# Kernel optimization log

Measured on AMD Instinct MI355X. Metric: run time of the kernel, lower is better.

## Reference

```python
import jax, jax.numpy as jnp
import numpy as np

DIM = 768
NUM_HEADS = 12
HEAD_DIM = DIM // NUM_HEADS
SCALE = HEAD_DIM ** -0.5
EPS = 1e-6


def setup_inputs() -> dict:
    key = jax.random.key(0)
    k_x, k_p, k_qkv, k_proj = jax.random.split(key, 4)
    B, N = 16, 577
    x = jax.random.normal(k_x, (B, N, DIM), dtype=jnp.float32)
    # binary keep/drop policy per token (as produced by an upstream gumbel gate)
    policy = jax.random.randint(k_p, (B, N, 1), 0, 2).astype(jnp.float32)
    Wqkv = jax.random.normal(k_qkv, (DIM, 3 * DIM), dtype=jnp.float32) * 0.02
    bqkv = jnp.zeros((3 * DIM,), dtype=jnp.float32)
    Wproj = jax.random.normal(k_proj, (DIM, DIM), dtype=jnp.float32) * 0.02
    bproj = jnp.zeros((DIM,), dtype=jnp.float32)
    return {"x": x, "policy": policy, "Wqkv": Wqkv, "bqkv": bqkv,
            "Wproj": Wproj, "bproj": bproj}


def reference(x, policy, Wqkv, bqkv, Wproj, bproj):
    B, N, C = x.shape
    # qkv projection -> [3, B, H, N, Dh]
    qkv = (x @ Wqkv + bqkv).reshape(B, N, 3, NUM_HEADS, HEAD_DIM)
    qkv = jnp.transpose(qkv, (2, 0, 3, 1, 4))
    q, k, v = qkv[0], qkv[1], qkv[2]
    # scaled attention logits [B, H, N, N]
    attn = jnp.einsum("bhnd,bhmd->bhnm", q, k) * SCALE
    # policy-masked softmax (training-mode formula: eye keeps self-attention alive)
    ap = policy.reshape(B, 1, 1, N)
    eye = jnp.eye(N, dtype=ap.dtype).reshape(1, 1, N, N)
    ap = ap + (1.0 - ap) * eye
    max_att = jnp.max(attn, axis=-1, keepdims=True)
    e = jnp.exp(attn - max_att) * ap
    attn = (e + EPS / N) / (jnp.sum(e, axis=-1, keepdims=True) + EPS)
    # attend and project
    out = jnp.einsum("bhnm,bhmd->bhnd", attn, v)
    out = jnp.transpose(out, (0, 2, 1, 3)).reshape(B, N, C)
    return out @ Wproj + bproj
```

## Files before the change

kernel.cpp:

```cpp
#include <hip/hip_runtime.h>
#include <hip/hip_bf16.h>

#define QKVC   2304
#define NHEAD  12
#define NTOK   577
#define NBATCH 16
#define NROWS  (NBATCH * NTOK)
#define NPAD   640
#define SCALE  0.125f
#define EPSV   1e-6f
#define KT     24
#define CH     512

typedef __bf16  bf16x8 __attribute__((ext_vector_type(8)));
typedef float   f32x4  __attribute__((ext_vector_type(4)));

__device__ __forceinline__ unsigned short f2bf(float f) {
    union { float f; unsigned u; } v; v.f = f;
    unsigned r = v.u + 0x7FFFu + ((v.u >> 16) & 1u);
    return (unsigned short)(r >> 16);
}
__device__ __forceinline__ unsigned short f2bf_trunc(float f) {
    return (unsigned short)(__float_as_uint(f) >> 16);
}
__device__ __forceinline__ unsigned pack2bf(float a, float b) {
    return (unsigned)f2bf(a) | ((unsigned)f2bf(b) << 16);
}
__device__ __forceinline__ f32x4 mfma16(bf16x8 a, bf16x8 b, f32x4 c) {
    return __builtin_amdgcn_mfma_f32_16x16x32_bf16(a, b, c, 0, 0, 0);
}

#define GLDS16(g, l) __builtin_amdgcn_global_load_lds( \
    (const __attribute__((address_space(1))) unsigned int*)(g), \
    (__attribute__((address_space(3))) unsigned int*)(l), 16, 0, 0)


__device__ void transpose_tile(const float* __restrict__ src, unsigned short* __restrict__ dst,
                               int N, int bx, int by, int t) {
    __shared__ unsigned short lt[64 * 72];
    int n0 = bx * 64, k0 = by * 64;
    int kk = t >> 4, nn = (t & 15) * 4;
    for (int i = 0; i < 4; i++) {
        int kr = kk + i * 16;
        float4 v = *(const float4*)&src[(size_t)(k0 + kr) * N + n0 + nn];
        lt[(nn + 0) * 72 + kr] = f2bf(v.x);
        lt[(nn + 1) * 72 + kr] = f2bf(v.y);
        lt[(nn + 2) * 72 + kr] = f2bf(v.z);
        lt[(nn + 3) * 72 + kr] = f2bf(v.w);
    }
    __syncthreads();
    int n = t >> 2;
    int ks = (t & 3) * 16;
    int gn = n0 + n;
    int ntile = gn >> 4, r = gn & 15, s = (r >> 1) & 3;
    for (int j = 0; j < 2; j++) {
        int k = k0 + ks + j * 8;
        int kt = k >> 5;
        int q = ((k >> 3) & 3) ^ s;
        uint4 v = *(uint4*)&lt[n * 72 + ks + j * 8];
        *(uint4*)&dst[((size_t)ntile * KT + kt) * CH + r * 32 + q * 8] = v;
    }
}

#define NCHUNK (577 * KT)
#define CONVB  ((NCHUNK + 15) / 16)
__global__ void k_prep(const float* __restrict__ x, unsigned short* __restrict__ xbt,
                       const float* __restrict__ Wqkv, unsigned short* __restrict__ wqkvt,
                       const float* __restrict__ Wproj, unsigned short* __restrict__ wprojt) {
    int id = blockIdx.x, t = threadIdx.x;
    if (id < CONVB) {
        int cid = id * 16 + (t >> 4);
        if (cid < NCHUNK) {
            int r = t & 15;
            int mt = cid / KT, kt = cid - mt * KT;
            const float* src = x + ((size_t)mt * 16 + r) * 768 + kt * 32;
            int s = (r >> 1) & 3;
            unsigned short* dst = xbt + (size_t)cid * CH + r * 32;
            #pragma unroll
            for (int q = 0; q < 4; q++) {
                int g = q ^ s;
                float4 v0 = *(const float4*)(src + g * 8);
                float4 v1 = *(const float4*)(src + g * 8 + 4);
                uint4 u;
                u.x = pack2bf(v0.x, v0.y);
                u.y = pack2bf(v0.z, v0.w);
                u.z = pack2bf(v1.x, v1.y);
                u.w = pack2bf(v1.z, v1.w);
                *(uint4*)(dst + q * 8) = u;
            }
        }
    } else if (id < CONVB + 432) {
        int i2 = id - CONVB;
        transpose_tile(Wqkv, wqkvt, QKVC, i2 % 36, i2 / 36, t);
    } else {
        int i2 = id - CONVB - 432;
        transpose_tile(Wproj, wprojt, 768, i2 % 12, i2 / 12, t);
    }
}

template <bool F32OUT>
__global__ __launch_bounds__(512, 2)
void k_gemm(const unsigned short* __restrict__ A, const unsigned short* __restrict__ B,
            const float* __restrict__ bias, void* __restrict__ outp, int Ncols,
            unsigned short* __restrict__ vt) {
    __shared__ unsigned short SL[36864];
    int t = threadIdx.x;
    int lane = t & 63, wave = t >> 6, quad = lane >> 4, l15 = lane & 15;
    int wm = wave >> 2, wn = wave & 3;
    int nT = Ncols >> 7;
    int nwg = gridDim.x;

    int q8 = nwg >> 3, r8 = nwg & 7;
    int xcd = blockIdx.x & 7, idx = blockIdx.x >> 3;
    int wg = (xcd < r8 ? xcd * (q8 + 1) : r8 * (q8 + 1) + (xcd - r8) * q8) + idx;
    int m0 = (wg / nT) * 256;
    int n0 = (wg % nT) * 128;

    const unsigned short* gA0 = A + ((size_t)((m0 >> 4) + wave) * KT) * CH + lane * 8;
    const unsigned short* gA1 = gA0 + (size_t)8 * KT * CH;
    const unsigned short* gB0 = B + ((size_t)((n0 >> 4) + wave) * KT) * CH + lane * 8;

    f32x4 acc[8][2] = {};

    auto STAGE = [&](int sx, unsigned slot) {
        unsigned sa = slot * 8192u + (unsigned)wave * 512u;
        unsigned sb = 24576u + slot * 4096u + (unsigned)wave * 512u;
        GLDS16(gA0 + sx * CH, &SL[sa]);
        GLDS16(gA1 + sx * CH, &SL[sa + 4096]);
        GLDS16(gB0 + sx * CH, &SL[sb]);
    };

    unsigned ro = (unsigned)(quad ^ ((l15 >> 1) & 3)) * 8u;

    auto STEP = [&](unsigned slot, int sx, unsigned sslot, bool stage) {
        unsigned ab = slot * 8192u;
        unsigned bb = 24576u + slot * 4096u;
        if (stage) STAGE(sx, sslot);
        bf16x8 b0 = *(const bf16x8*)&SL[bb + (unsigned)(wn * 32 + l15) * 32u + ro];
        bf16x8 b1 = *(const bf16x8*)&SL[bb + (unsigned)(wn * 32 + 16 + l15) * 32u + ro];
        __builtin_amdgcn_s_setprio(1);
        #pragma unroll
        for (int mi = 0; mi < 8; mi++) {
            bf16x8 a = *(const bf16x8*)&SL[ab + (unsigned)(wm * 128 + mi * 16 + l15) * 32u + ro];
            acc[mi][0] = mfma16(a, b0, acc[mi][0]);
            acc[mi][1] = mfma16(a, b1, acc[mi][1]);
        }
        __builtin_amdgcn_s_setprio(0);
    };

    STAGE(0, 0); STAGE(1, 1);
    for (int s = 0; s < 23; s++) {
        asm volatile("s_waitcnt vmcnt(3)" ::: "memory");
        asm volatile("s_barrier" ::: "memory");
        STEP((unsigned)(s % 3), s + 2, (unsigned)((s + 2) % 3), s < 22);
    }
    asm volatile("s_waitcnt vmcnt(0)" ::: "memory");
    asm volatile("s_barrier" ::: "memory");
    STEP(2u, 0, 0u, false);

    if constexpr (F32OUT) {
        for (int ni = 0; ni < 2; ni++) {
            int col = n0 + wn * 32 + ni * 16 + l15;
            float bv = bias[col];
            for (int mi = 0; mi < 8; mi++) {
                int rowm = m0 + wm * 128 + mi * 16 + quad * 4;
                for (int r = 0; r < 4; r++) {
                    int m = rowm + r;
                    if (m < NROWS)
                        ((float*)outp)[(size_t)m * Ncols + col] = acc[mi][ni][r] + bv;
                }
            }
        }
    } else {
        __syncthreads();
        for (int ni = 0; ni < 2; ni++) {
            int colL = wn * 32 + ni * 16 + l15;
            float bv = bias[n0 + colL];
            for (int mi = 0; mi < 8; mi++) {
                int rowL = wm * 128 + mi * 16 + quad * 4;
                for (int r = 0; r < 4; r++)
                    SL[(rowL + r) * 136 + colL] = f2bf(acc[mi][ni][r] + bv);
            }
        }
        __syncthreads();
        if (n0 < 1536) {
            for (int rr = 0; rr < 8; rr++) {
                int row = rr * 32 + (t >> 4);
                int m = m0 + row;
                if (m < NROWS) {
                    uint4 v = *(uint4*)&SL[row * 136 + (t & 15) * 8];
                    *(uint4*)&((unsigned short*)outp)[(size_t)m * Ncols + n0 + (t & 15) * 8] = v;
                }
            }
        } else {
            int h0 = (n0 - 1536) >> 6;
            for (int i = 0; i < 16; i++) {
                int c = wave * 16 + i;
                int h = h0 + (c >> 6), d = c & 63;
                for (int half = 0; half < 4; half++) {
                    int lr = half * 64 + lane;
                    int m = m0 + lr;
                    if (m < NROWS) {
                        unsigned bbx = (unsigned)m / 577u;
                        int tok = m - (int)bbx * 577;
                        vt[(((size_t)bbx * NHEAD + h) * 64 + d) * NPAD + tok] =
                            SL[lr * 136 + c];
                    }
                }
            }
        }
    }
}

__global__ __launch_bounds__(256, 4)
void k_attn(const unsigned short* __restrict__ qkv, const unsigned short* __restrict__ vt,
            const float* __restrict__ policy, unsigned short* __restrict__ ao) {
    __shared__ unsigned short Ks[64 * 72];
    __shared__ unsigned short Vs[64 * 72];
    __shared__ unsigned short Ps[4][32 * 72];
    __shared__ float pol[NPAD];
    int t = threadIdx.x;
    int lane = t & 63, wave = t >> 6, quad = lane >> 4, l15 = lane & 15;
    int b = blockIdx.z, h = blockIdx.y, qt = blockIdx.x;
    const unsigned short* qbase = qkv + (size_t)(b * NTOK) * QKVC + h * 64;
    const unsigned short* kbase = qkv + (size_t)(b * NTOK) * QKVC + 768 + h * 64;
    const unsigned short* vbase = vt + (size_t)(b * NHEAD + h) * 64 * NPAD;

    for (int i = t; i < NPAD; i += 256)
        pol[i] = (i < NTOK) ? policy[b * NTOK + i] : 0.f;

    bf16x8 qf[2][2];
    for (int mi = 0; mi < 2; mi++) {
        const unsigned short* qp =
            qbase + (size_t)(qt * 128 + mi * 64 + wave * 16 + l15) * QKVC + quad * 8;
        qf[mi][0] = *(const bf16x8*)qp;
        qf[mi][1] = *(const bf16x8*)(qp + 32);
    }
    bf16x8 onesf;
    for (int j = 0; j < 8; j++) onesf[j] = (__bf16)1.0f;
    f32x4 o[2][4] = {};
    f32x4 ls[2] = {};
    int rowtok0[2];
    for (int mi = 0; mi < 2; mi++)
        rowtok0[mi] = qt * 128 + mi * 64 + wave * 16 + quad * 4;
    __syncthreads();

    for (int kt = 0; kt < 10; kt++) {
        int key0 = kt * 64;
        for (int i = t; i < 512; i += 256) {
            int row = i >> 3, seg = (i & 7) * 8;
            *(uint4*)&Ks[row * 72 + seg] = *(const uint4*)&kbase[(size_t)(key0 + row) * QKVC + seg];
            *(uint4*)&Vs[row * 72 + seg] = *(const uint4*)&vbase[(size_t)row * NPAD + key0 + seg];
        }
        __syncthreads();

        for (int ci = 0; ci < 4; ci++) {
            bf16x8 kf0 = *(const bf16x8*)&Ks[(ci * 16 + l15) * 72 + quad * 8];
            bf16x8 kf1 = *(const bf16x8*)&Ks[(ci * 16 + l15) * 72 + 32 + quad * 8];
            int col = key0 + ci * 16 + l15;
            float pc = pol[col];
            for (int mi = 0; mi < 2; mi++) {
                f32x4 a = {};
                a = mfma16(qf[mi][0], kf0, a);
                a = mfma16(qf[mi][1], kf1, a);
                for (int r = 0; r < 4; r++) {
                    float ap = (col == rowtok0[mi] + r) ? 1.f : pc;
                    float e = __expf(a[r] * SCALE) * ap;
                    Ps[wave][(mi * 16 + quad * 4 + r) * 72 + ci * 16 + l15] = f2bf_trunc(e);
                }
            }
        }
        __asm__ volatile("s_waitcnt lgkmcnt(0)" ::: "memory");
        bf16x8 pf[2][2];
        for (int mi = 0; mi < 2; mi++) {
            pf[mi][0] = *(const bf16x8*)&Ps[wave][(mi * 16 + l15) * 72 + quad * 8];
            pf[mi][1] = *(const bf16x8*)&Ps[wave][(mi * 16 + l15) * 72 + 32 + quad * 8];
            ls[mi] = mfma16(pf[mi][0], onesf, ls[mi]);
            ls[mi] = mfma16(pf[mi][1], onesf, ls[mi]);
        }
        for (int di = 0; di < 4; di++) {
            bf16x8 vf0 = *(const bf16x8*)&Vs[(di * 16 + l15) * 72 + quad * 8];
            bf16x8 vf1 = *(const bf16x8*)&Vs[(di * 16 + l15) * 72 + 32 + quad * 8];
            for (int mi = 0; mi < 2; mi++) {
                o[mi][di] = mfma16(pf[mi][0], vf0, o[mi][di]);
                o[mi][di] = mfma16(pf[mi][1], vf1, o[mi][di]);
            }
        }
        __syncthreads();
    }

    for (int mi = 0; mi < 2; mi++) {
        for (int r = 0; r < 4; r++) {
            int tok = rowtok0[mi] + r;
            if (tok < NTOK) {
                float inv = __builtin_amdgcn_rcpf(ls[mi][r] + EPSV);
                int m = b * NTOK + tok;
                int mt = m >> 4, rr = m & 15, s = (rr >> 1) & 3;
                unsigned short* dst = ao + ((size_t)mt * KT) * CH + rr * 32;
                for (int di = 0; di < 4; di++) {
                    int k = h * 64 + di * 16 + l15;
                    int kt2 = k >> 5;
                    int q = ((k >> 3) & 3) ^ s;
                    dst[(size_t)kt2 * CH + q * 8 + (l15 & 7)] =
                        f2bf(o[mi][di][r] * inv);
                }
            }
        }
    }
}

extern "C" void kernel_launch(void* const* d_in, const int* in_sizes, int n_in,
                              void* d_out, int out_size, void* d_ws, size_t ws_size,
                              hipStream_t stream) {
    const float* x      = (const float*)d_in[0];
    const float* policy = (const float*)d_in[1];
    const float* Wqkv   = (const float*)d_in[2];
    const float* bqkv   = (const float*)d_in[3];
    const float* Wproj  = (const float*)d_in[4];
    const float* bproj  = (const float*)d_in[5];
    float* out = (float*)d_out;

    unsigned short* p = (unsigned short*)d_ws;
    unsigned short* xb     = p;
    unsigned short* ao     = p; p += (size_t)NROWS * 768;
    unsigned short* wqkvt  = p; p += (size_t)QKVC * 768;
    unsigned short* wprojt = p; p += (size_t)768 * 768;
    unsigned short* qkvb   = p; p += (size_t)NROWS * QKVC;
    unsigned short* vt     = p; p += (size_t)NBATCH * NHEAD * 64 * NPAD;

    int mT = (NROWS + 255) / 256;

    k_prep<<<CONVB + 432 + 144, 256, 0, stream>>>(x, xb, Wqkv, wqkvt, Wproj, wprojt);
    k_gemm<false><<<mT * (QKVC / 128), 512, 0, stream>>>(
        xb, wqkvt, bqkv, (void*)qkvb, QKVC, vt);
    k_attn<<<dim3(NPAD / 128, NHEAD, NBATCH), 256, 0, stream>>>(qkvb, vt, policy, ao);
    k_gemm<true><<<mT * (768 / 128), 512, 0, stream>>>(
        ao, wprojt, bproj, (void*)out, 768, nullptr);
}
```

Measured before the change: 193.1 us.

## Enlarge GEMM tile to 256x256 with 4-phase split-K double-buffered pipeline

The GEMM block tile grows from 256x128 to 256x256, with K staged two sub-chunks at a time into 128KB of double-buffered LDS. Each K step is split into four quadrant phases that interleave global-to-LDS prefetch with MFMA work. The aim is to raise arithmetic intensity and halve B/A reload traffic per output. In exchange the block uses the full LDS and more accumulators, which drops occupancy to one block per CU, and the grid gets smaller, which may hurt load balance (the projection GEMM has only 3 column tiles).

```diff
diff --git a/kernel.cpp b/kernel.cpp
--- a/kernel.cpp
+++ b/kernel.cpp
@@ -103,108 +103,145 @@
 void k_gemm(const unsigned short* __restrict__ A, const unsigned short* __restrict__ B,
             const float* __restrict__ bias, void* __restrict__ outp, int Ncols,
             unsigned short* __restrict__ vt) {
-    __shared__ unsigned short SL[36864];
+    __shared__ unsigned short SL[65536];
     int t = threadIdx.x;
     int lane = t & 63, wave = t >> 6, quad = lane >> 4, l15 = lane & 15;
     int wm = wave >> 2, wn = wave & 3;
-    int nT = Ncols >> 7;
+    int nT = Ncols >> 8;
     int nwg = gridDim.x;
 
     int q8 = nwg >> 3, r8 = nwg & 7;
     int xcd = blockIdx.x & 7, idx = blockIdx.x >> 3;
     int wg = (xcd < r8 ? xcd * (q8 + 1) : r8 * (q8 + 1) + (xcd - r8) * q8) + idx;
     int m0 = (wg / nT) * 256;
-    int n0 = (wg % nT) * 128;
-
-    const unsigned short* gA0 = A + ((size_t)((m0 >> 4) + wave) * KT) * CH + lane * 8;
-    const unsigned short* gA1 = gA0 + (size_t)8 * KT * CH;
-    const unsigned short* gB0 = B + ((size_t)((n0 >> 4) + wave) * KT) * CH + lane * 8;
-
-    f32x4 acc[8][2] = {};
-
-    auto STAGE = [&](int sx, unsigned slot) {
-        unsigned sa = slot * 8192u + (unsigned)wave * 512u;
-        unsigned sb = 24576u + slot * 4096u + (unsigned)wave * 512u;
-        GLDS16(gA0 + sx * CH, &SL[sa]);
-        GLDS16(gA1 + sx * CH, &SL[sa + 4096]);
-        GLDS16(gB0 + sx * CH, &SL[sb]);
+    int n0 = (wg % nT) * 256;
+
+    unsigned ro = (unsigned)(quad ^ ((l15 >> 1) & 3)) * 8u;
+
+    int mwA = (wave & 3) + 8 * (wave >> 2);
+    int nwB = (wave & 1) + 4 * (wave >> 1);
+
+    auto SA = [&](int mh, int tau) {
+        int ml = 4 * mh + mwA;
+        unsigned dst = (unsigned)(tau & 1) * 16384u + (unsigned)ml * 1024u;
+        const unsigned short* g =
+            A + ((size_t)((m0 >> 4) + ml) * KT + tau * 2) * CH + lane * 8;
+        GLDS16(g,      &SL[dst]);
+        GLDS16(g + CH, &SL[dst + 512]);
     };
-
-    unsigned ro = (unsigned)(quad ^ ((l15 >> 1) & 3)) * 8u;
-
-    auto STEP = [&](unsigned slot, int sx, unsigned sslot, bool stage) {
-        unsigned ab = slot * 8192u;
-        unsigned bb = 24576u + slot * 4096u;
-        if (stage) STAGE(sx, sslot);
-        bf16x8 b0 = *(const bf16x8*)&SL[bb + (unsigned)(wn * 32 + l15) * 32u + ro];
-        bf16x8 b1 = *(const bf16x8*)&SL[bb + (unsigned)(wn * 32 + 16 + l15) * 32u + ro];
+    auto SB = [&](int nh, int tau) {
+        int nl = 2 * nh + nwB;
+        unsigned dst = 32768u + (unsigned)(tau & 1) * 16384u + (unsigned)nl * 1024u;
+        const unsigned short* g =
+            B + ((size_t)((n0 >> 4) + nl) * KT + tau * 2) * CH + lane * 8;
+        GLDS16(g,      &SL[dst]);
+        GLDS16(g + CH, &SL[dst + 512]);
+    };
+
+    f32x4 acc[8][4] = {};
+
+    auto PHASE = [&](int tau, int mh, int nh) {
+        unsigned ab = (unsigned)(tau & 1) * 16384u;
+        unsigned bb = 32768u + ab;
+        bf16x8 af[4][2], bfr[2][2];
+        #pragma unroll
+        for (int i = 0; i < 4; i++) {
+            unsigned mo = ab + (unsigned)(wm * 8 + 4 * mh + i) * 1024u + l15 * 32u + ro;
+            af[i][0] = *(const bf16x8*)&SL[mo];
+            af[i][1] = *(const bf16x8*)&SL[mo + 512u];
+        }
+        #pragma unroll
+        for (int j = 0; j < 2; j++) {
+            unsigned no = bb + (unsigned)(wn * 4 + 2 * nh + j) * 1024u + l15 * 32u + ro;
+            bfr[j][0] = *(const bf16x8*)&SL[no];
+            bfr[j][1] = *(const bf16x8*)&SL[no + 512u];
+        }
+        int p = mh * 2 + nh;
+        if      (p == 0) { if (tau + 1 < 12) SA(1, tau + 1); }
+        else if (p == 1) { if (tau + 1 < 12) SB(1, tau + 1); }
+        else if (p == 2) { if (tau + 2 < 12) SA(0, tau + 2); }
+        else             { if (tau + 2 < 12) SB(0, tau + 2); }
+        asm volatile("s_barrier" ::: "memory");
         __builtin_amdgcn_s_setprio(1);
         #pragma unroll
-        for (int mi = 0; mi < 8; mi++) {
-            bf16x8 a = *(const bf16x8*)&SL[ab + (unsigned)(wm * 128 + mi * 16 + l15) * 32u + ro];
-            acc[mi][0] = mfma16(a, b0, acc[mi][0]);
-            acc[mi][1] = mfma16(a, b1, acc[mi][1]);
-        }
+        for (int i = 0; i < 4; i++)
+            #pragma unroll
+            for (int j = 0; j < 2; j++) {
+                acc[4*mh+i][2*nh+j] = mfma16(af[i][0], bfr[j][0], acc[4*mh+i][2*nh+j]);
+                acc[4*mh+i][2*nh+j] = mfma16(af[i][1], bfr[j][1], acc[4*mh+i][2*nh+j]);
+            }
         __builtin_amdgcn_s_setprio(0);
+        if (p == 0) {
+            if (tau == 11) asm volatile("s_waitcnt vmcnt(0)" ::: "memory");
+            else           asm volatile("s_waitcnt vmcnt(6)" ::: "memory");
+        } else if (p == 3) {
+            if (tau == 10)     asm volatile("s_waitcnt vmcnt(4)" ::: "memory");
+            else if (tau < 10) asm volatile("s_waitcnt vmcnt(8)" ::: "memory");
+        }
+        asm volatile("s_barrier" ::: "memory");
     };
 
-    STAGE(0, 0); STAGE(1, 1);
-    for (int s = 0; s < 23; s++) {
-        asm volatile("s_waitcnt vmcnt(3)" ::: "memory");
-        asm volatile("s_barrier" ::: "memory");
-        STEP((unsigned)(s % 3), s + 2, (unsigned)((s + 2) % 3), s < 22);
-    }
-    asm volatile("s_waitcnt vmcnt(0)" ::: "memory");
+    SA(0, 0); SB(0, 0); SA(1, 0); SB(1, 0); SA(0, 1); SB(0, 1);
+    asm volatile("s_waitcnt vmcnt(8)" ::: "memory");
     asm volatile("s_barrier" ::: "memory");
-    STEP(2u, 0, 0u, false);
+
+    for (int tau = 0; tau < 12; tau++) {
+        PHASE(tau, 0, 0); PHASE(tau, 0, 1); PHASE(tau, 1, 0); PHASE(tau, 1, 1);
+    }
 
     if constexpr (F32OUT) {
-        for (int ni = 0; ni < 2; ni++) {
-            int col = n0 + wn * 32 + ni * 16 + l15;
+        #pragma unroll
+        for (int j = 0; j < 4; j++) {
+            int col = n0 + wn * 64 + j * 16 + l15;
             float bv = bias[col];
-            for (int mi = 0; mi < 8; mi++) {
-                int rowm = m0 + wm * 128 + mi * 16 + quad * 4;
+            for (int i = 0; i < 8; i++) {
+                int rowm = m0 + wm * 128 + i * 16 + quad * 4;
                 for (int r = 0; r < 4; r++) {
                     int m = rowm + r;
                     if (m < NROWS)
-                        ((float*)outp)[(size_t)m * Ncols + col] = acc[mi][ni][r] + bv;
+                        ((float*)outp)[(size_t)m * Ncols + col] = acc[i][j][r] + bv;
                 }
             }
         }
     } else {
-        __syncthreads();
-        for (int ni = 0; ni < 2; ni++) {
-            int colL = wn * 32 + ni * 16 + l15;
-            float bv = bias[n0 + colL];
-            for (int mi = 0; mi < 8; mi++) {
-                int rowL = wm * 128 + mi * 16 + quad * 4;
-                for (int r = 0; r < 4; r++)
-                    SL[(rowL + r) * 136 + colL] = f2bf(acc[mi][ni][r] + bv);
-            }
-        }
-        __syncthreads();
-        if (n0 < 1536) {
-            for (int rr = 0; rr < 8; rr++) {
-                int row = rr * 32 + (t >> 4);
-                int m = m0 + row;
-                if (m < NROWS) {
-                    uint4 v = *(uint4*)&SL[row * 136 + (t & 15) * 8];
-                    *(uint4*)&((unsigned short*)outp)[(size_t)m * Ncols + n0 + (t & 15) * 8] = v;
-                }
-            }
-        } else {
-            int h0 = (n0 - 1536) >> 6;
-            for (int i = 0; i < 16; i++) {
-                int c = wave * 16 + i;
-                int h = h0 + (c >> 6), d = c & 63;
-                for (int half = 0; half < 4; half++) {
-                    int lr = half * 64 + lane;
-                    int m = m0 + lr;
+        for (int h = 0; h < 2; h++) {
+            __syncthreads();
+            if ((wn >> 1) == h) {
+                for (int j = 0; j < 4; j++) {
+                    int colL = (wn & 1) * 64 + j * 16 + l15;
+                    float bv = bias[n0 + h * 128 + colL];
+                    for (int i = 0; i < 8; i++) {
+                        int rowL = wm * 128 + i * 16 + quad * 4;
+                        for (int r = 0; r < 4; r++)
+                            SL[(rowL + r) * 136 + colL] = f2bf(acc[i][j][r] + bv);
+                    }
+                }
+            }
+            __syncthreads();
+            int n0h = n0 + h * 128;
+            if (n0h < 1536) {
+                for (int rr = 0; rr < 8; rr++) {
+                    int row = rr * 32 + (t >> 4);
+                    int m = m0 + row;
                     if (m < NROWS) {
-                        unsigned bbx = (unsigned)m / 577u;
-                        int tok = m - (int)bbx * 577;
-                        vt[(((size_t)bbx * NHEAD + h) * 64 + d) * NPAD + tok] =
-                            SL[lr * 136 + c];
+                        uint4 v = *(uint4*)&SL[row * 136 + (t & 15) * 8];
+                        *(uint4*)&((unsigned short*)outp)[(size_t)m * Ncols + n0h + (t & 15) * 8] = v;
+                    }
+                }
+            } else {
+                int h0 = (n0h - 1536) >> 6;
+                for (int i2 = 0; i2 < 16; i2++) {
+                    int c = wave * 16 + i2;
+                    int hh = h0 + (c >> 6), d = c & 63;
+                    for (int half = 0; half < 4; half++) {
+                        int lr = half * 64 + lane;
+                        int m = m0 + lr;
+                        if (m < NROWS) {
+                            unsigned bbx = (unsigned)m / 577u;
+                            int tok = m - (int)bbx * 577;
+                            vt[(((size_t)bbx * NHEAD + hh) * 64 + d) * NPAD + tok] =
+                                SL[lr * 136 + c];
+                        }
                     }
                 }
             }
@@ -331,9 +368,9 @@
     int mT = (NROWS + 255) / 256;
 
     k_prep<<<CONVB + 432 + 144, 256, 0, stream>>>(x, xb, Wqkv, wqkvt, Wproj, wprojt);
-    k_gemm<false><<<mT * (QKVC / 128), 512, 0, stream>>>(
+    k_gemm<false><<<mT * (QKVC / 256), 512, 0, stream>>>(
         xb, wqkvt, bqkv, (void*)qkvb, QKVC, vt);
     k_attn<<<dim3(NPAD / 128, NHEAD, NBATCH), 256, 0, stream>>>(qkvb, vt, policy, ao);
-    k_gemm<true><<<mT * (768 / 128), 512, 0, stream>>>(
+    k_gemm<true><<<mT * (768 / 256), 512, 0, stream>>>(
         ao, wprojt, bproj, (void*)out, 768, nullptr);
 }
```

After: 237.4 us. 22.9% more time.
